# Performance work log

Measured on AMD Instinct MI355X. Metric: run time of the kernel, lower is better.

Reference implementation:

```python
import jax, jax.numpy as jnp
import numpy as np

NUM_NODES = 80000
V_GLOBALS = 50000
N = 32      # grapharea_size
D = 300     # feature dim
R = 4       # num relations
E = 64      # edges per timestep
B, T = 2, 64


def setup_inputs() -> dict:
    key = jax.random.key(0)
    ks = jax.random.split(key, 10)
    return {
        "x_indices": jax.random.randint(ks[0], (B, T, N), 0, NUM_NODES, dtype=jnp.int32),
        "edge_index": jax.random.randint(ks[1], (B, T, 2, E), 0, N, dtype=jnp.int32),
        "edge_type": jax.random.randint(ks[2], (B, T, E), 0, R, dtype=jnp.int32),
        "X": jax.random.normal(ks[3], (NUM_NODES, D), jnp.float32) * 0.1,
        "conv_W": jax.random.normal(ks[4], (R, D, D), jnp.float32) * (1.0 / np.sqrt(D)),
        "W_0": jax.random.normal(ks[5], (D, D), jnp.float32) * (1.0 / np.sqrt(D)),
        "update_gate_W": jax.random.normal(ks[6], (N * D, D), jnp.float32) * (1.0 / np.sqrt(N * D)),
        "update_gate_U": jax.random.normal(ks[7], (D, D), jnp.float32) * (1.0 / np.sqrt(D)),
        "lin_w": jax.random.normal(ks[8], (V_GLOBALS, D), jnp.float32) * (1.0 / np.sqrt(D)),
        "lin_b": jax.random.normal(ks[9], (V_GLOBALS,), jnp.float32) * 0.01,
    }


def _rgcn_step(X, conv_W, W_0, Wg, Ug, lin_w, lin_b, mem, idx, ei, et):
    # gather grapharea features: [N, D]
    gx = X[idx]
    src, dst = ei[0], ei[1]
    n = gx.shape[0]
    r = conv_W.shape[0]
    # per-relation linear transform: [R, N, D]
    xw = jnp.einsum('nd,rde->rne', gx, conv_W)
    # edge-type masks emulate split_edge_index: [R, E]
    mask = (et[None, :] == jnp.arange(r, dtype=et.dtype)[:, None]).astype(gx.dtype)
    # GCN symmetric normalization with self-loops (deg includes self-loop weight 1)
    deg = jax.vmap(lambda w: jax.ops.segment_sum(w, dst, num_segments=n))(mask) + 1.0  # [R, N]
    dis = jax.lax.rsqrt(deg)
    norm = dis[:, src] * dis[:, dst] * mask                      # [R, E]
    msgs = xw[:, src, :] * norm[..., None]                       # [R, E, D]
    agg = jax.vmap(lambda m: jax.ops.segment_sum(m, dst, num_segments=n))(msgs)
    agg = agg + xw * (dis ** 2)[..., None]                       # self-loop messages
    composite = agg.sum(0)                                       # sum over relations, [N, D]
    # eye(N) @ (gx @ W_0) == gx @ W_0
    proposed = composite + gx @ W_0
    # GRU-style update gate from flattened grapharea + previous memory's first node
    u = jax.nn.sigmoid(gx.reshape(-1) @ Wg + mem[0] @ Ug)        # [D]
    new = u[None, :] * proposed + (1.0 - u[None, :]) * mem       # [N, D]
    x1 = jax.nn.leaky_relu(new)[0]                               # current node, [D]
    logits = x1 @ lin_w.T + lin_b                                # [V]
    return new, jax.nn.log_softmax(logits)


def reference(x_indices, edge_index, edge_type, X, conv_W, W_0, update_gate_W, update_gate_U, lin_w, lin_b):
    b, t, n = x_indices.shape
    s = b * t
    idxs = x_indices.reshape(s, n)
    eis = edge_index.reshape(s, 2, -1)
    ets = edge_type.reshape(s, -1)

    def step(mem, inp):
        idx, ei, et = inp
        new, logp = _rgcn_step(X, conv_W, W_0, update_gate_W, update_gate_U,
                               lin_w, lin_b, mem, idx, ei, et)
        # memory carry is a non-grad buffer updated via .data.copy_ in torch
        return jax.lax.stop_gradient(new), logp

    mem0 = jnp.zeros((n, X.shape[1]), X.dtype)
    _, preds_globals = jax.lax.scan(step, mem0, (idxs, eis, ets))  # [S, V]
    preds_senses = jnp.zeros((s,), X.dtype)  # include_senses=False -> stacked zeros
    return preds_globals, preds_senses
```

## Files before the change

kernel.cpp:

```cpp
#include <hip/hip_runtime.h>

#define S 128
#define N 32
#define D 300
#define DP 320
#define E 64
#define R 4
#define V 50000
#define VP 50048
#define ND 9600
#define KY 1504
#define DPAD 304

typedef unsigned short ushortT;
typedef __attribute__((ext_vector_type(8))) short short8;
typedef __attribute__((ext_vector_type(4))) short short4v;
typedef __attribute__((ext_vector_type(4))) float floatx4;
typedef __attribute__((ext_vector_type(2))) _Float16 half2v;
typedef __attribute__((ext_vector_type(13))) unsigned int uintx13;

#if defined(__has_builtin)
#if __has_builtin(__builtin_amdgcn_fdot2)
#define HAVE_FDOT2 1
#endif
#endif

__device__ inline float bf2f(ushortT h) {
    unsigned u = ((unsigned)h) << 16;
    float f;
    __builtin_memcpy(&f, &u, 4);
    return f;
}

__device__ inline float bfbits_lo(unsigned u) {
    unsigned b = u << 16;
    float f;
    __builtin_memcpy(&f, &b, 4);
    return f;
}

__device__ inline float bfbits_hi(unsigned u) {
    unsigned b = u & 0xffff0000u;
    float f;
    __builtin_memcpy(&f, &b, 4);
    return f;
}

__device__ inline ushortT f2bf(float f) {
    unsigned u;
    __builtin_memcpy(&u, &f, 4);
    unsigned r = (u + 0x7fffu + ((u >> 16) & 1u)) >> 16;
    return (ushortT)r;
}

__device__ inline float ldf(const void* p, size_t i, int isb) {
    return isb ? bf2f(((const ushortT*)p)[i]) : ((const float*)p)[i];
}

__device__ inline float dot2f(unsigned a, unsigned b, float c) {
    half2v av, bv;
    __builtin_memcpy(&av, &a, 4);
    __builtin_memcpy(&bv, &b, 4);
#if defined(HAVE_FDOT2)
    return __builtin_amdgcn_fdot2(av, bv, c, false);
#else
    return fmaf((float)av[1], (float)bv[1], fmaf((float)av[0], (float)bv[0], c));
#endif
}

__device__ inline unsigned packh2(float lo, float hi) {
    half2v h;
    h[0] = (_Float16)lo;
    h[1] = (_Float16)hi;
    unsigned u;
    __builtin_memcpy(&u, &h, 4);
    return u;
}

__global__ void k_detect(const void* X, int* flag) {
    __shared__ int bad;
    if (threadIdx.x == 0) bad = 0;
    __syncthreads();
    const ushortT* p = (const ushortT*)X;
    int b = 0;
    for (int i = threadIdx.x; i < 4096; i += 256) {
        float v = bf2f(p[i]);
        if (!(v > -2.f && v < 2.f)) b = 1;
    }
    if (b) atomicOr(&bad, 1);
    __syncthreads();
    if (threadIdx.x == 0) flag[0] = bad ? 0 : 1;
}

__global__ void k_gatherb(const int* __restrict__ flag, const int* __restrict__ xi,
                          const void* __restrict__ X, ushortT* __restrict__ gxb) {
    int isb = flag[0];
    int sn = blockIdx.x;
    int d = threadIdx.x;
    if (d < D) {
        int node = xi[sn];
        ushortT v = isb ? ((const ushortT*)X)[(size_t)node * D + d]
                        : f2bf(((const float*)X)[(size_t)node * D + d]);
        gxb[(size_t)sn * D + d] = v;
    }
}

__global__ void k_twg(const int* __restrict__ flag, const void* __restrict__ Wg,
                      ushortT* __restrict__ wgt) {
    int isb = flag[0];
    __shared__ float tile[32][33];
    int k0 = blockIdx.x * 32, d0 = blockIdx.y * 32;
    int tx = threadIdx.x & 31, ty = threadIdx.x >> 5;
    for (int i = ty; i < 32; i += 8) {
        int d = d0 + tx;
        tile[i][tx] = (d < D) ? ldf(Wg, (size_t)(k0 + i) * D + d, isb) : 0.f;
    }
    __syncthreads();
    for (int i = ty; i < 32; i += 8) {
        int d = d0 + i;
        if (d < DPAD) wgt[(size_t)d * ND + k0 + tx] = f2bf(tile[tx][i]);
    }
}

__global__ void k_tws(const int* __restrict__ flag, const void* __restrict__ convW,
                      const void* __restrict__ W0, ushortT* __restrict__ wst) {
    int isb = flag[0];
    __shared__ float tile[32][33];
    int k0 = blockIdx.x * 32, d0 = blockIdx.y * 32;
    int tx = threadIdx.x & 31, ty = threadIdx.x >> 5;
    for (int i = ty; i < 32; i += 8) {
        int kp = k0 + i, d = d0 + tx;
        float v = 0.f;
        if (d < D && kp < 1500)
            v = (kp < 1200) ? ldf(convW, (size_t)kp * D + d, isb)
                            : ldf(W0, (size_t)(kp - 1200) * D + d, isb);
        tile[i][tx] = v;
    }
    __syncthreads();
    for (int i = ty; i < 32; i += 8) {
        int d = d0 + i;
        if (d < DPAD) wst[(size_t)d * KY + k0 + tx] = f2bf(tile[tx][i]);
    }
}

__global__ void k_yb(const ushortT* __restrict__ gxb, const int* __restrict__ ei,
                     const int* __restrict__ et, ushortT* __restrict__ yb) {
    int s = blockIdx.x;
    int t = threadIdx.x;
    __shared__ int se[E], de[E], te[E];
    __shared__ float disv[R][N];
    if (t < E) {
        se[t] = ei[(size_t)s * 2 * E + t];
        de[t] = ei[(size_t)s * 2 * E + E + t];
        te[t] = et[(size_t)s * E + t];
    }
    __syncthreads();
    if (t < R * N) {
        int r = t >> 5, n = t & 31;
        float c = 1.f;
        for (int e = 0; e < E; ++e) c += (te[e] == r && de[e] == n) ? 1.f : 0.f;
        disv[r][n] = rsqrtf(c);
    }
    __syncthreads();
    if (t < D) {
        const ushortT* g = gxb + (size_t)s * ND;
        float g0 = bf2f(g[t]);
        float yy[R];
#pragma unroll
        for (int r = 0; r < R; ++r) yy[r] = g0 * disv[r][0] * disv[r][0];
        for (int e = 0; e < E; ++e) {
            if (de[e] == 0) {
                int r = te[e];
                yy[r] += disv[r][se[e]] * disv[r][0] * bf2f(g[(size_t)se[e] * D + t]);
            }
        }
#pragma unroll
        for (int r = 0; r < R; ++r) yb[(size_t)s * KY + r * D + t] = f2bf(yy[r]);
        yb[(size_t)s * KY + 4 * D + t] = g[t];
    }
    if (t < 4) yb[(size_t)s * KY + 1500 + t] = 0;
}

__global__ __launch_bounds__(256) void k_gemm(const ushortT* __restrict__ A, int lda,
                                              const ushortT* __restrict__ Bt, int ldb,
                                              float* __restrict__ C, int ldc, int ncols,
                                              int kchunks, int per) {
    int wave = threadIdx.x >> 6, lane = threadIdx.x & 63;
    int col = lane & 15, quad = lane >> 4;
    int m0 = blockIdx.x * 16, n0 = blockIdx.y * 16;
    int z = blockIdx.z;
    int kbeg = z * per;
    int kend = kbeg + per;
    if (kend > kchunks) kend = kchunks;
    floatx4 acc = {0.f, 0.f, 0.f, 0.f};
    const ushortT* ap = A + (size_t)(m0 + col) * lda + quad * 8;
    const ushortT* bp = Bt + (size_t)(n0 + col) * ldb + quad * 8;
    for (int kc = kbeg + wave; kc < kend; kc += 4) {
        short8 a = *(const short8*)(ap + kc * 32);
        short8 b = *(const short8*)(bp + kc * 32);
        acc = __builtin_amdgcn_mfma_f32_16x16x32_bf16(a, b, acc, 0, 0, 0);
    }
    __shared__ float red[4][64][4];
#pragma unroll
    for (int i = 0; i < 4; ++i) red[wave][lane][i] = acc[i];
    __syncthreads();
    if (wave == 0) {
#pragma unroll
        for (int i = 0; i < 4; ++i) {
            float v = red[0][lane][i] + red[1][lane][i] + red[2][lane][i] + red[3][lane][i];
            int m = m0 + quad * 4 + i;
            int n = n0 + col;
            if (n < ncols) C[(size_t)z * S * ldc + (size_t)m * ldc + n] = v;
        }
    }
}

__global__ void k_red(const float* __restrict__ part, float* __restrict__ out, int n, int nz) {
    int i = blockIdx.x * 256 + threadIdx.x;
    if (i < n) {
        float v = 0.f;
        for (int z = 0; z < nz; ++z) v += part[(size_t)z * n + i];
        out[i] = v;
    }
}

__global__ __attribute__((amdgpu_flat_work_group_size(768, 768), amdgpu_waves_per_eu(2, 2))) void
k_scan(const int* __restrict__ flag, const float* __restrict__ a, const float* __restrict__ P0,
       const void* __restrict__ Ug, ushortT* __restrict__ x1p) {
    int isb = flag[0];
    int t = threadIdx.x;
    int w = t >> 6, lane = t & 63;
    int kbase = w * 25;
    int myk = kbase + lane;
    bool red_ok = lane < 25;
    int d4 = 256 + lane;
    bool d4ok = d4 < D;
    uintx13 UV0, UV1, UV2, UV3, UV4;
#pragma unroll
    for (int j = 0; j < 13; ++j) {
        int k1 = kbase + 2 * j, k2 = k1 + 1;
        bool k2ok = (2 * j + 1) < 25;
        UV0[j] = packh2(ldf(Ug, (size_t)k1 * D + lane, isb),
                        k2ok ? ldf(Ug, (size_t)k2 * D + lane, isb) : 0.f);
        UV1[j] = packh2(ldf(Ug, (size_t)k1 * D + 64 + lane, isb),
                        k2ok ? ldf(Ug, (size_t)k2 * D + 64 + lane, isb) : 0.f);
        UV2[j] = packh2(ldf(Ug, (size_t)k1 * D + 128 + lane, isb),
                        k2ok ? ldf(Ug, (size_t)k2 * D + 128 + lane, isb) : 0.f);
        UV3[j] = packh2(ldf(Ug, (size_t)k1 * D + 192 + lane, isb),
                        k2ok ? ldf(Ug, (size_t)k2 * D + 192 + lane, isb) : 0.f);
        UV4[j] = packh2(d4ok ? ldf(Ug, (size_t)k1 * D + d4, isb) : 0.f,
                        (k2ok && d4ok) ? ldf(Ug, (size_t)k2 * D + d4, isb) : 0.f);
    }
    for (int i = t; i < S * 20; i += 768) {
        int s = i / 20, d = 300 + (i % 20);
        x1p[(size_t)s * DP + d] = 0;
    }
    __shared__ float part[2][12][320];
    __shared__ unsigned msh16[12 * 13];
    for (int i = t; i < 12 * 13; i += 768) msh16[i] = 0;
    float mreg = 0.f;
    int buf = 0;
    float av = 0.f, pv = 0.f;
    if (red_ok) {
        av = a[myk];
        pv = P0[myk];
    }
    __syncthreads();
    for (int s = 0; s < S; ++s) {
        float avn = 0.f, pvn = 0.f;
        if (red_ok && s + 1 < S) {
            avn = a[(size_t)(s + 1) * D + myk];
            pvn = P0[(size_t)(s + 1) * D + myk];
        }
        uintx13 MV;
#pragma unroll
        for (int j = 0; j < 13; ++j) MV[j] = msh16[13 * w + j];
        float acc0 = 0.f, acc1 = 0.f, acc2 = 0.f, acc3 = 0.f, acc4 = 0.f;
#pragma unroll
        for (int j = 0; j < 13; ++j) {
            unsigned md = MV[j];
            acc0 = dot2f(UV0[j], md, acc0);
            acc1 = dot2f(UV1[j], md, acc1);
            acc2 = dot2f(UV2[j], md, acc2);
            acc3 = dot2f(UV3[j], md, acc3);
            acc4 = dot2f(UV4[j], md, acc4);
        }
        part[buf][w][lane] = acc0;
        part[buf][w][64 + lane] = acc1;
        part[buf][w][128 + lane] = acc2;
        part[buf][w][192 + lane] = acc3;
        part[buf][w][256 + lane] = acc4;
        __syncthreads();
        if (red_ok) {
            float q0 = part[buf][0][myk] + part[buf][1][myk];
            float q1 = part[buf][2][myk] + part[buf][3][myk];
            float q2 = part[buf][4][myk] + part[buf][5][myk];
            float q3 = part[buf][6][myk] + part[buf][7][myk];
            float q4 = part[buf][8][myk] + part[buf][9][myk];
            float q5 = part[buf][10][myk] + part[buf][11][myk];
            float pr = av + (((q0 + q1) + (q2 + q3)) + (q4 + q5));
            float u = 1.f / (1.f + __expf(-pr));
            float nm = u * pv + (1.f - u) * mreg;
            mreg = nm;
            _Float16 mh = (_Float16)nm;
            ushortT mb;
            __builtin_memcpy(&mb, &mh, 2);
            ((ushortT*)msh16)[26 * w + lane] = mb;
            float x = nm > 0.f ? nm : 0.01f * nm;
            x1p[(size_t)s * DP + myk] = f2bf(x);
        }
        av = avn;
        pv = pvn;
        buf ^= 1;
    }
}

__global__ __launch_bounds__(256) void k_logits(const int* __restrict__ flag,
                                                const ushortT* __restrict__ x1p,
                                                const void* __restrict__ lw,
                                                const void* __restrict__ lb,
                                                void* __restrict__ out) {
    int isb = flag[0];
    int wave = threadIdx.x >> 6, lane = threadIdx.x & 63;
    int col = lane & 15, quad = lane >> 4;
    int v = blockIdx.x * 64 + wave * 16 + col;
    int vv = v < V ? v : V - 1;
    floatx4 acc[8];
#pragma unroll
    for (int i = 0; i < 8; ++i) acc[i] = (floatx4){0.f, 0.f, 0.f, 0.f};
#pragma unroll
    for (int kc = 0; kc < 9; ++kc) {
        int k0 = kc * 32 + quad * 8;
        short8 b;
        if (isb) {
            const ushortT* bp = (const ushortT*)lw + (size_t)vv * D + k0;
            short4v lo = *(const short4v*)bp;
            short4v hi = *(const short4v*)(bp + 4);
            b = (short8){lo[0], lo[1], lo[2], lo[3], hi[0], hi[1], hi[2], hi[3]};
        } else {
            const float* bp = (const float*)lw + (size_t)vv * D + k0;
            floatx4 f0 = *(const floatx4*)bp;
            floatx4 f1 = *(const floatx4*)(bp + 4);
            b = (short8){(short)f2bf(f0[0]), (short)f2bf(f0[1]), (short)f2bf(f0[2]),
                         (short)f2bf(f0[3]), (short)f2bf(f1[0]), (short)f2bf(f1[1]),
                         (short)f2bf(f1[2]), (short)f2bf(f1[3])};
        }
#pragma unroll
        for (int st = 0; st < 8; ++st) {
            short8 aa = *(const short8*)(x1p + (size_t)(st * 16 + col) * DP + k0);
            acc[st] = __builtin_amdgcn_mfma_f32_16x16x32_bf16(aa, b, acc[st], 0, 0, 0);
        }
    }
    {
        int k0 = 288 + quad * 8;
        short8 b;
#pragma unroll
        for (int j = 0; j < 8; ++j) {
            int k = k0 + j;
            ushortT bv = 0;
            if (k < D)
                bv = isb ? ((const ushortT*)lw)[(size_t)vv * D + k]
                         : f2bf(((const float*)lw)[(size_t)vv * D + k]);
            b[j] = (short)bv;
        }
#pragma unroll
        for (int st = 0; st < 8; ++st) {
            short8 aa = *(const short8*)(x1p + (size_t)(st * 16 + col) * DP + k0);
            acc[st] = __builtin_amdgcn_mfma_f32_16x16x32_bf16(aa, b, acc[st], 0, 0, 0);
        }
    }
    if (v < V) {
        float bias = ldf(lb, v, isb);
#pragma unroll
        for (int st = 0; st < 8; ++st) {
#pragma unroll
            for (int i = 0; i < 4; ++i) {
                int s = st * 16 + quad * 4 + i;
                float val = acc[st][i] + bias;
                if (isb)
                    ((ushortT*)out)[(size_t)s * V + v] = f2bf(val);
                else
                    ((float*)out)[(size_t)s * V + v] = val;
            }
        }
    }
}

__global__ __launch_bounds__(512) void k_norm(const int* __restrict__ flag,
                                              void* __restrict__ out) {
    int isb = flag[0];
    int s = blockIdx.x;
    int t = threadIdx.x;
    __shared__ float red[512];
    if (s == 0 && t < S) {
        if (isb)
            ((ushortT*)out)[(size_t)S * V + t] = 0;
        else
            ((float*)out)[(size_t)S * V + t] = 0.f;
    }
    float mx = -1e30f;
    if (isb) {
        const uint4* row = (const uint4*)((const ushortT*)out + (size_t)s * V);
        for (int i = t; i < 6250; i += 512) {
            uint4 q = row[i];
            mx = fmaxf(mx, fmaxf(fmaxf(bfbits_lo(q.x), bfbits_hi(q.x)),
                                 fmaxf(bfbits_lo(q.y), bfbits_hi(q.y))));
            mx = fmaxf(mx, fmaxf(fmaxf(bfbits_lo(q.z), bfbits_hi(q.z)),
                                 fmaxf(bfbits_lo(q.w), bfbits_hi(q.w))));
        }
    } else {
        const floatx4* row = (const floatx4*)((const float*)out + (size_t)s * V);
        for (int i = t; i < 12500; i += 512) {
            floatx4 q = row[i];
            mx = fmaxf(mx, fmaxf(fmaxf(q[0], q[1]), fmaxf(q[2], q[3])));
        }
    }
    red[t] = mx;
    __syncthreads();
    for (int o = 256; o > 0; o >>= 1) {
        if (t < o) red[t] = fmaxf(red[t], red[t + o]);
        __syncthreads();
    }
    float M = red[0];
    __syncthreads();
    float sm = 0.f;
    if (isb) {
        const uint4* row = (const uint4*)((const ushortT*)out + (size_t)s * V);
        for (int i = t; i < 6250; i += 512) {
            uint4 q = row[i];
            sm += __expf(bfbits_lo(q.x) - M) + __expf(bfbits_hi(q.x) - M) +
                  __expf(bfbits_lo(q.y) - M) + __expf(bfbits_hi(q.y) - M) +
                  __expf(bfbits_lo(q.z) - M) + __expf(bfbits_hi(q.z) - M) +
                  __expf(bfbits_lo(q.w) - M) + __expf(bfbits_hi(q.w) - M);
        }
    } else {
        const floatx4* row = (const floatx4*)((const float*)out + (size_t)s * V);
        for (int i = t; i < 12500; i += 512) {
            floatx4 q = row[i];
            sm += __expf(q[0] - M) + __expf(q[1] - M) + __expf(q[2] - M) + __expf(q[3] - M);
        }
    }
    red[t] = sm;
    __syncthreads();
    for (int o = 256; o > 0; o >>= 1) {
        if (t < o) red[t] += red[t + o];
        __syncthreads();
    }
    float lse = M + __logf(red[0]);
    if (isb) {
        uint4* row = (uint4*)((ushortT*)out + (size_t)s * V);
        for (int i = t; i < 6250; i += 512) {
            uint4 q = row[i];
            uint4 o;
            o.x = (unsigned)f2bf(bfbits_lo(q.x) - lse) |
                  ((unsigned)f2bf(bfbits_hi(q.x) - lse) << 16);
            o.y = (unsigned)f2bf(bfbits_lo(q.y) - lse) |
                  ((unsigned)f2bf(bfbits_hi(q.y) - lse) << 16);
            o.z = (unsigned)f2bf(bfbits_lo(q.z) - lse) |
                  ((unsigned)f2bf(bfbits_hi(q.z) - lse) << 16);
            o.w = (unsigned)f2bf(bfbits_lo(q.w) - lse) |
                  ((unsigned)f2bf(bfbits_hi(q.w) - lse) << 16);
            row[i] = o;
        }
    } else {
        floatx4* row = (floatx4*)((float*)out + (size_t)s * V);
        for (int i = t; i < 12500; i += 512) {
            floatx4 q = row[i];
            q[0] -= lse;
            q[1] -= lse;
            q[2] -= lse;
            q[3] -= lse;
            row[i] = q;
        }
    }
}

#define OFF_FLAG 0
#define OFF_GXB 256
#define OFF_WGT 2457856
#define OFF_WST 8294656
#define OFF_YB 9209088
#define OFF_A 9594112
#define OFF_P0 9747712
#define OFF_X1P 9901312
#define OFF_STATS 9983232
#define OFF_PART 9983744
#define PART_A_BYTES (4 * S * D * 4)
#define PART_P_BYTES (2 * S * D * 4)

extern "C" void kernel_launch(void* const* d_in, const int* in_sizes, int n_in, void* d_out,
                              int out_size, void* d_ws, size_t ws_size, hipStream_t stream) {
    const int* xi = (const int*)d_in[0];
    const int* ei = (const int*)d_in[1];
    const int* et = (const int*)d_in[2];
    const void* X = d_in[3];
    const void* convW = d_in[4];
    const void* W0 = d_in[5];
    const void* Wg = d_in[6];
    const void* Ug = d_in[7];
    const void* lw = d_in[8];
    const void* lb = d_in[9];
    char* ws = (char*)d_ws;

    int* flag = (int*)(ws + OFF_FLAG);
    ushortT* gxb = (ushortT*)(ws + OFF_GXB);
    ushortT* wgt = (ushortT*)(ws + OFF_WGT);
    ushortT* wst = (ushortT*)(ws + OFF_WST);
    ushortT* yb = (ushortT*)(ws + OFF_YB);
    float* a = (float*)(ws + OFF_A);
    float* P0 = (float*)(ws + OFF_P0);
    ushortT* x1p = (ushortT*)(ws + OFF_X1P);

    bool split = ws_size >= (size_t)(OFF_PART + PART_A_BYTES + PART_P_BYTES);
    int nza = split ? 4 : 1;
    int nzp = split ? 2 : 1;
    float* apart = split ? (float*)(ws + OFF_PART) : a;
    float* ppart = split ? (float*)(ws + OFF_PART + PART_A_BYTES) : P0;
    int pera = (ND / 32 + nza - 1) / nza;
    int perp = (KY / 32 + nzp - 1) / nzp;

    hipLaunchKernelGGL(k_detect, dim3(1), dim3(256), 0, stream, X, flag);
    hipLaunchKernelGGL(k_gatherb, dim3(S * N), dim3(DP), 0, stream, flag, xi, X, gxb);
    hipLaunchKernelGGL(k_twg, dim3(ND / 32, 10), dim3(256), 0, stream, flag, Wg, wgt);
    hipLaunchKernelGGL(k_tws, dim3(KY / 32, 10), dim3(256), 0, stream, flag, convW, W0, wst);
    hipLaunchKernelGGL(k_yb, dim3(S), dim3(DP), 0, stream, gxb, ei, et, yb);
    hipLaunchKernelGGL(k_gemm, dim3(S / 16, 19, nza), dim3(256), 0, stream, gxb, ND, wgt, ND,
                       apart, D, D, ND / 32, pera);
    if (split)
        hipLaunchKernelGGL(k_red, dim3((S * D + 255) / 256), dim3(256), 0, stream, apart, a,
                           S * D, nza);
    hipLaunchKernelGGL(k_gemm, dim3(S / 16, 19, nzp), dim3(256), 0, stream, yb, KY, wst, KY,
                       ppart, D, D, KY / 32, perp);
    if (split)
        hipLaunchKernelGGL(k_red, dim3((S * D + 255) / 256), dim3(256), 0, stream, ppart, P0,
                           S * D, nzp);
    hipLaunchKernelGGL(k_scan, dim3(1), dim3(768), 0, stream, flag, a, P0, Ug, x1p);
    hipLaunchKernelGGL(k_logits, dim3(VP / 64), dim3(256), 0, stream, flag, x1p, lw, lb, d_out);
    hipLaunchKernelGGL(k_norm, dim3(S), dim3(512), 0, stream, flag, d_out);
}
```

Baseline: 426.3 us.

## Fuse prep, gather, GEMM and reduction kernels; use readlane for scan memory broadcast

Merges the two weight-transpose kernels into one launch and fuses the feature gather into the yb kernel through a shared-memory tile. The two split-K GEMMs run as a single launch, and the separate split-K reduction kernels are removed by summing the partials inside the sequential scan's prefetch. Inside the scan, each lane handles two features and the memory vector is broadcast via readlane instead of shared memory. The aim is to cut launch count and serial latency per scan step. The trade-off is extra partial loads in the serial scan loop and less parallelism in the gather, which now uses 128 blocks instead of 4096.

Result: slower. 837.0 us (+96.3%).

```diff
diff --git a/kernel.cpp b/kernel.cpp
--- a/kernel.cpp
+++ b/kernel.cpp
@@ -16,6 +16,7 @@
 typedef __attribute__((ext_vector_type(8))) short short8;
 typedef __attribute__((ext_vector_type(4))) short short4v;
 typedef __attribute__((ext_vector_type(4))) float floatx4;
+typedef __attribute__((ext_vector_type(2))) float floatx2;
 typedef __attribute__((ext_vector_type(2))) _Float16 half2v;
 typedef __attribute__((ext_vector_type(13))) unsigned int uintx13;
 
@@ -55,6 +56,10 @@
 
 __device__ inline float ldf(const void* p, size_t i, int isb) {
     return isb ? bf2f(((const ushortT*)p)[i]) : ((const float*)p)[i];
+}
+
+__device__ inline unsigned rdlaneu(unsigned v, int lane) {
+    return (unsigned)__builtin_amdgcn_readlane((int)v, lane);
 }
 
 __device__ inline float dot2f(unsigned a, unsigned b, float c) {
@@ -77,6 +82,32 @@
     return u;
 }
 
+__device__ inline void ldred(const float* base, int s, int d1, bool pair, int nz,
+                             float& v1, float& v2) {
+    v1 = 0.f;
+    v2 = 0.f;
+    for (int z = 0; z < nz; ++z) {
+        const float* p = base + ((size_t)z * S + s) * D + d1;
+        if (pair) {
+            floatx2 q = *(const floatx2*)p;
+            v1 += q[0];
+            v2 += q[1];
+        } else {
+            v1 += *p;
+        }
+    }
+}
+
+__device__ inline float tree12(const float* pb, int d) {
+    float q0 = pb[0 * 320 + d] + pb[1 * 320 + d];
+    float q1 = pb[2 * 320 + d] + pb[3 * 320 + d];
+    float q2 = pb[4 * 320 + d] + pb[5 * 320 + d];
+    float q3 = pb[6 * 320 + d] + pb[7 * 320 + d];
+    float q4 = pb[8 * 320 + d] + pb[9 * 320 + d];
+    float q5 = pb[10 * 320 + d] + pb[11 * 320 + d];
+    return ((q0 + q1) + (q2 + q3)) + (q4 + q5);
+}
+
 __global__ void k_detect(const void* X, int* flag) {
     __shared__ int bad;
     if (threadIdx.x == 0) bad = 0;
@@ -92,61 +123,51 @@
     if (threadIdx.x == 0) flag[0] = bad ? 0 : 1;
 }
 
-__global__ void k_gatherb(const int* __restrict__ flag, const int* __restrict__ xi,
-                          const void* __restrict__ X, ushortT* __restrict__ gxb) {
-    int isb = flag[0];
-    int sn = blockIdx.x;
-    int d = threadIdx.x;
-    if (d < D) {
-        int node = xi[sn];
-        ushortT v = isb ? ((const ushortT*)X)[(size_t)node * D + d]
-                        : f2bf(((const float*)X)[(size_t)node * D + d]);
-        gxb[(size_t)sn * D + d] = v;
-    }
-}
-
-__global__ void k_twg(const int* __restrict__ flag, const void* __restrict__ Wg,
-                      ushortT* __restrict__ wgt) {
+__global__ void k_prep(const int* __restrict__ flag, const void* __restrict__ Wg,
+                       const void* __restrict__ convW, const void* __restrict__ W0,
+                       ushortT* __restrict__ wgt, ushortT* __restrict__ wst) {
     int isb = flag[0];
     __shared__ float tile[32][33];
-    int k0 = blockIdx.x * 32, d0 = blockIdx.y * 32;
+    int bx = blockIdx.x;
+    int d0 = blockIdx.y * 32;
     int tx = threadIdx.x & 31, ty = threadIdx.x >> 5;
-    for (int i = ty; i < 32; i += 8) {
-        int d = d0 + tx;
-        tile[i][tx] = (d < D) ? ldf(Wg, (size_t)(k0 + i) * D + d, isb) : 0.f;
-    }
-    __syncthreads();
-    for (int i = ty; i < 32; i += 8) {
-        int d = d0 + i;
-        if (d < DPAD) wgt[(size_t)d * ND + k0 + tx] = f2bf(tile[tx][i]);
-    }
-}
-
-__global__ void k_tws(const int* __restrict__ flag, const void* __restrict__ convW,
-                      const void* __restrict__ W0, ushortT* __restrict__ wst) {
+    if (bx < ND / 32) {
+        int k0 = bx * 32;
+        for (int i = ty; i < 32; i += 8) {
+            int d = d0 + tx;
+            tile[i][tx] = (d < D) ? ldf(Wg, (size_t)(k0 + i) * D + d, isb) : 0.f;
+        }
+        __syncthreads();
+        for (int i = ty; i < 32; i += 8) {
+            int d = d0 + i;
+            if (d < DPAD) wgt[(size_t)d * ND + k0 + tx] = f2bf(tile[tx][i]);
+        }
+    } else {
+        int k0 = (bx - ND / 32) * 32;
+        for (int i = ty; i < 32; i += 8) {
+            int kp = k0 + i, d = d0 + tx;
+            float v = 0.f;
+            if (d < D && kp < 1500)
+                v = (kp < 1200) ? ldf(convW, (size_t)kp * D + d, isb)
+                                : ldf(W0, (size_t)(kp - 1200) * D + d, isb);
+            tile[i][tx] = v;
+        }
+        __syncthreads();
+        for (int i = ty; i < 32; i += 8) {
+            int d = d0 + i;
+            if (d < DPAD) wst[(size_t)d * KY + k0 + tx] = f2bf(tile[tx][i]);
+        }
+    }
+}
+
+__global__ void k_gyb(const int* __restrict__ flag, const int* __restrict__ xi,
+                      const void* __restrict__ X, const int* __restrict__ ei,
+                      const int* __restrict__ et, ushortT* __restrict__ gxb,
+                      ushortT* __restrict__ yb) {
     int isb = flag[0];
-    __shared__ float tile[32][33];
-    int k0 = blockIdx.x * 32, d0 = blockIdx.y * 32;
-    int tx = threadIdx.x & 31, ty = threadIdx.x >> 5;
-    for (int i = ty; i < 32; i += 8) {
-        int kp = k0 + i, d = d0 + tx;
-        float v = 0.f;
-        if (d < D && kp < 1500)
-            v = (kp < 1200) ? ldf(convW, (size_t)kp * D + d, isb)
-                            : ldf(W0, (size_t)(kp - 1200) * D + d, isb);
-        tile[i][tx] = v;
-    }
-    __syncthreads();
-    for (int i = ty; i < 32; i += 8) {
-        int d = d0 + i;
-        if (d < DPAD) wst[(size_t)d * KY + k0 + tx] = f2bf(tile[tx][i]);
-    }
-}
-
-__global__ void k_yb(const ushortT* __restrict__ gxb, const int* __restrict__ ei,
-                     const int* __restrict__ et, ushortT* __restrict__ yb) {
     int s = blockIdx.x;
     int t = threadIdx.x;
+    __shared__ ushortT gl[N][D];
     __shared__ int se[E], de[E], te[E];
     __shared__ float disv[R][N];
     if (t < E) {
@@ -154,6 +175,16 @@
         de[t] = ei[(size_t)s * 2 * E + E + t];
         te[t] = et[(size_t)s * E + t];
     }
+    if (t < D) {
+#pragma unroll 4
+        for (int r = 0; r < N; ++r) {
+            int node = xi[s * N + r];
+            ushortT v = isb ? ((const ushortT*)X)[(size_t)node * D + t]
+                            : f2bf(((const float*)X)[(size_t)node * D + t]);
+            gl[r][t] = v;
+            gxb[(size_t)(s * N + r) * D + t] = v;
+        }
+    }
     __syncthreads();
     if (t < R * N) {
         int r = t >> 5, n = t & 31;
@@ -163,38 +194,49 @@
     }
     __syncthreads();
     if (t < D) {
-        const ushortT* g = gxb + (size_t)s * ND;
-        float g0 = bf2f(g[t]);
+        float g0 = bf2f(gl[0][t]);
         float yy[R];
 #pragma unroll
         for (int r = 0; r < R; ++r) yy[r] = g0 * disv[r][0] * disv[r][0];
         for (int e = 0; e < E; ++e) {
             if (de[e] == 0) {
                 int r = te[e];
-                yy[r] += disv[r][se[e]] * disv[r][0] * bf2f(g[(size_t)se[e] * D + t]);
+                yy[r] += disv[r][se[e]] * disv[r][0] * bf2f(gl[se[e]][t]);
             }
         }
 #pragma unroll
         for (int r = 0; r < R; ++r) yb[(size_t)s * KY + r * D + t] = f2bf(yy[r]);
-        yb[(size_t)s * KY + 4 * D + t] = g[t];
+        yb[(size_t)s * KY + 4 * D + t] = gl[0][t];
     }
     if (t < 4) yb[(size_t)s * KY + 1500 + t] = 0;
 }
 
-__global__ __launch_bounds__(256) void k_gemm(const ushortT* __restrict__ A, int lda,
-                                              const ushortT* __restrict__ Bt, int ldb,
-                                              float* __restrict__ C, int ldc, int ncols,
-                                              int kchunks, int per) {
+__global__ __launch_bounds__(256) void k_gemm2(const ushortT* __restrict__ gxb,
+                                               const ushortT* __restrict__ wgt,
+                                               const ushortT* __restrict__ yb,
+                                               const ushortT* __restrict__ wst,
+                                               float* __restrict__ apart,
+                                               float* __restrict__ ppart, int nza, int nzp) {
     int wave = threadIdx.x >> 6, lane = threadIdx.x & 63;
     int col = lane & 15, quad = lane >> 4;
     int m0 = blockIdx.x * 16, n0 = blockIdx.y * 16;
     int z = blockIdx.z;
-    int kbeg = z * per;
+    const ushortT *A, *Bt;
+    float* C;
+    int ld, kchunks, per, zz;
+    if (z < nza) {
+        A = gxb; Bt = wgt; C = apart; ld = ND; kchunks = ND / 32;
+        zz = z; per = (kchunks + nza - 1) / nza;
+    } else {
+        A = yb; Bt = wst; C = ppart; ld = KY; kchunks = KY / 32;
+        zz = z - nza; per = (kchunks + nzp - 1) / nzp;
+    }
+    int kbeg = zz * per;
     int kend = kbeg + per;
     if (kend > kchunks) kend = kchunks;
     floatx4 acc = {0.f, 0.f, 0.f, 0.f};
-    const ushortT* ap = A + (size_t)(m0 + col) * lda + quad * 8;
-    const ushortT* bp = Bt + (size_t)(n0 + col) * ldb + quad * 8;
+    const ushortT* ap = A + (size_t)(m0 + col) * ld + quad * 8;
+    const ushortT* bp = Bt + (size_t)(n0 + col) * ld + quad * 8;
     for (int kc = kbeg + wave; kc < kend; kc += 4) {
         short8 a = *(const short8*)(ap + kc * 32);
         short8 b = *(const short8*)(bp + kc * 32);
@@ -210,29 +252,19 @@
             float v = red[0][lane][i] + red[1][lane][i] + red[2][lane][i] + red[3][lane][i];
             int m = m0 + quad * 4 + i;
             int n = n0 + col;
-            if (n < ncols) C[(size_t)z * S * ldc + (size_t)m * ldc + n] = v;
-        }
-    }
-}
-
-__global__ void k_red(const float* __restrict__ part, float* __restrict__ out, int n, int nz) {
-    int i = blockIdx.x * 256 + threadIdx.x;
-    if (i < n) {
-        float v = 0.f;
-        for (int z = 0; z < nz; ++z) v += part[(size_t)z * n + i];
-        out[i] = v;
+            if (n < D) C[(size_t)zz * S * D + (size_t)m * D + n] = v;
+        }
     }
 }
 
 __global__ __attribute__((amdgpu_flat_work_group_size(768, 768), amdgpu_waves_per_eu(2, 2))) void
-k_scan(const int* __restrict__ flag, const float* __restrict__ a, const float* __restrict__ P0,
-       const void* __restrict__ Ug, ushortT* __restrict__ x1p) {
+k_scan(const int* __restrict__ flag, const float* __restrict__ apart,
+       const float* __restrict__ ppart, int nza, int nzp, const void* __restrict__ Ug,
+       ushortT* __restrict__ x1p) {
     int isb = flag[0];
     int t = threadIdx.x;
     int w = t >> 6, lane = t & 63;
     int kbase = w * 25;
-    int myk = kbase + lane;
-    bool red_ok = lane < 25;
     int d4 = 256 + lane;
     bool d4ok = d4 < D;
     uintx13 UV0, UV1, UV2, UV3, UV4;
@@ -256,25 +288,26 @@
         x1p[(size_t)s * DP + d] = 0;
     }
     __shared__ float part[2][12][320];
-    __shared__ unsigned msh16[12 * 13];
-    for (int i = t; i < 12 * 13; i += 768) msh16[i] = 0;
-    float mreg = 0.f;
+    bool jok = lane < 13;
+    bool pair = lane < 12;
+    int d1 = kbase + 2 * lane;
+    float m1 = 0.f, m2 = 0.f;
+    unsigned mpack = 0;
     int buf = 0;
-    float av = 0.f, pv = 0.f;
-    if (red_ok) {
-        av = a[myk];
-        pv = P0[myk];
-    }
-    __syncthreads();
+    float av1 = 0.f, av2 = 0.f, pv1 = 0.f, pv2 = 0.f;
+    if (jok) {
+        ldred(apart, 0, d1, pair, nza, av1, av2);
+        ldred(ppart, 0, d1, pair, nzp, pv1, pv2);
+    }
     for (int s = 0; s < S; ++s) {
-        float avn = 0.f, pvn = 0.f;
-        if (red_ok && s + 1 < S) {
-            avn = a[(size_t)(s + 1) * D + myk];
-            pvn = P0[(size_t)(s + 1) * D + myk];
+        float an1 = 0.f, an2 = 0.f, pn1 = 0.f, pn2 = 0.f;
+        if (jok && s + 1 < S) {
+            ldred(apart, s + 1, d1, pair, nza, an1, an2);
+            ldred(ppart, s + 1, d1, pair, nzp, pn1, pn2);
         }
         uintx13 MV;
 #pragma unroll
-        for (int j = 0; j < 13; ++j) MV[j] = msh16[13 * w + j];
+        for (int j = 0; j < 13; ++j) MV[j] = rdlaneu(mpack, j);
         float acc0 = 0.f, acc1 = 0.f, acc2 = 0.f, acc3 = 0.f, acc4 = 0.f;
 #pragma unroll
         for (int j = 0; j < 13; ++j) {
@@ -291,26 +324,28 @@
         part[buf][w][192 + lane] = acc3;
         part[buf][w][256 + lane] = acc4;
         __syncthreads();
-        if (red_ok) {
-            float q0 = part[buf][0][myk] + part[buf][1][myk];
-            float q1 = part[buf][2][myk] + part[buf][3][myk];
-            float q2 = part[buf][4][myk] + part[buf][5][myk];
-            float q3 = part[buf][6][myk] + part[buf][7][myk];
-            float q4 = part[buf][8][myk] + part[buf][9][myk];
-            float q5 = part[buf][10][myk] + part[buf][11][myk];
-            float pr = av + (((q0 + q1) + (q2 + q3)) + (q4 + q5));
-            float u = 1.f / (1.f + __expf(-pr));
-            float nm = u * pv + (1.f - u) * mreg;
-            mreg = nm;
-            _Float16 mh = (_Float16)nm;
-            ushortT mb;
-            __builtin_memcpy(&mb, &mh, 2);
-            ((ushortT*)msh16)[26 * w + lane] = mb;
-            float x = nm > 0.f ? nm : 0.01f * nm;
-            x1p[(size_t)s * DP + myk] = f2bf(x);
-        }
-        av = avn;
-        pv = pvn;
+        if (jok) {
+            const float* pb = &part[buf][0][0];
+            float pr1 = av1 + tree12(pb, d1);
+            float u1 = 1.f / (1.f + __expf(-pr1));
+            float nm1 = u1 * pv1 + (1.f - u1) * m1;
+            m1 = nm1;
+            float x1v = nm1 > 0.f ? nm1 : 0.01f * nm1;
+            if (pair) {
+                float pr2 = av2 + tree12(pb, d1 + 1);
+                float u2 = 1.f / (1.f + __expf(-pr2));
+                float nm2 = u2 * pv2 + (1.f - u2) * m2;
+                m2 = nm2;
+                mpack = packh2(nm1, nm2);
+                float x2v = nm2 > 0.f ? nm2 : 0.01f * nm2;
+                unsigned xw = (unsigned)f2bf(x1v) | ((unsigned)f2bf(x2v) << 16);
+                *(unsigned*)(x1p + (size_t)s * DP + d1) = xw;
+            } else {
+                mpack = packh2(nm1, 0.f);
+                x1p[(size_t)s * DP + d1] = f2bf(x1v);
+            }
+        }
+        av1 = an1; av2 = an2; pv1 = pn1; pv2 = pn2;
         buf ^= 1;
     }
 }
@@ -516,25 +551,15 @@
     int nzp = split ? 2 : 1;
     float* apart = split ? (float*)(ws + OFF_PART) : a;
     float* ppart = split ? (float*)(ws + OFF_PART + PART_A_BYTES) : P0;
-    int pera = (ND / 32 + nza - 1) / nza;
-    int perp = (KY / 32 + nzp - 1) / nzp;
 
     hipLaunchKernelGGL(k_detect, dim3(1), dim3(256), 0, stream, X, flag);
-    hipLaunchKernelGGL(k_gatherb, dim3(S * N), dim3(DP), 0, stream, flag, xi, X, gxb);
-    hipLaunchKernelGGL(k_twg, dim3(ND / 32, 10), dim3(256), 0, stream, flag, Wg, wgt);
-    hipLaunchKernelGGL(k_tws, dim3(KY / 32, 10), dim3(256), 0, stream, flag, convW, W0, wst);
-    hipLaunchKernelGGL(k_yb, dim3(S), dim3(DP), 0, stream, gxb, ei, et, yb);
-    hipLaunchKernelGGL(k_gemm, dim3(S / 16, 19, nza), dim3(256), 0, stream, gxb, ND, wgt, ND,
-                       apart, D, D, ND / 32, pera);
-    if (split)
-        hipLaunchKernelGGL(k_red, dim3((S * D + 255) / 256), dim3(256), 0, stream, apart, a,
-                           S * D, nza);
-    hipLaunchKernelGGL(k_gemm, dim3(S / 16, 19, nzp), dim3(256), 0, stream, yb, KY, wst, KY,
-                       ppart, D, D, KY / 32, perp);
-    if (split)
-        hipLaunchKernelGGL(k_red, dim3((S * D + 255) / 256), dim3(256), 0, stream, ppart, P0,
-                           S * D, nzp);
-    hipLaunchKernelGGL(k_scan, dim3(1), dim3(768), 0, stream, flag, a, P0, Ug, x1p);
+    hipLaunchKernelGGL(k_prep, dim3(ND / 32 + KY / 32, 10), dim3(256), 0, stream, flag, Wg,
+                       convW, W0, wgt, wst);
+    hipLaunchKernelGGL(k_gyb, dim3(S), dim3(DP), 0, stream, flag, xi, X, ei, et, gxb, yb);
+    hipLaunchKernelGGL(k_gemm2, dim3(S / 16, 19, nza + nzp), dim3(256), 0, stream, gxb, wgt,
+                       yb, wst, apart, ppart, nza, nzp);
+    hipLaunchKernelGGL(k_scan, dim3(1), dim3(768), 0, stream, flag, apart, ppart, nza, nzp,
+                       Ug, x1p);
     hipLaunchKernelGGL(k_logits, dim3(VP / 64), dim3(256), 0, stream, flag, x1p, lw, lb, d_out);
     hipLaunchKernelGGL(k_norm, dim3(S), dim3(512), 0, stream, flag, d_out);
 }
```

## Merge preprocessing, gather and GEMM launches; replace scan syncthreads with raw barrier

Applied to the files above, without the earlier changes.

Combines the two weight-transpose kernels into one launch, fuses the node-feature gather into the yb construction kernel (staging gathered rows in LDS), runs both split-K GEMMs in a single launch along the z dimension, and merges the two partial-sum reductions. This cuts the number of kernel launches and the inter-kernel gaps, and lets the yb step read features from LDS instead of global memory. In the serial scan kernel, __syncthreads is replaced by an explicit lgkmcnt wait plus s_barrier with scheduling fences, which may trim barrier overhead inside the per-step loop. The fused gather now runs on only 128 blocks instead of 4096, which could reduce parallelism for that gather.

New measurement: 423.9 us. Within noise of the previous version (-0.6%).

```diff
diff --git a/kernel.cpp b/kernel.cpp
--- a/kernel.cpp
+++ b/kernel.cpp
@@ -16,6 +16,7 @@
 typedef __attribute__((ext_vector_type(8))) short short8;
 typedef __attribute__((ext_vector_type(4))) short short4v;
 typedef __attribute__((ext_vector_type(4))) float floatx4;
+typedef __attribute__((ext_vector_type(2))) float floatx2;
 typedef __attribute__((ext_vector_type(2))) _Float16 half2v;
 typedef __attribute__((ext_vector_type(13))) unsigned int uintx13;
 
@@ -92,61 +93,51 @@
     if (threadIdx.x == 0) flag[0] = bad ? 0 : 1;
 }
 
-__global__ void k_gatherb(const int* __restrict__ flag, const int* __restrict__ xi,
-                          const void* __restrict__ X, ushortT* __restrict__ gxb) {
-    int isb = flag[0];
-    int sn = blockIdx.x;
-    int d = threadIdx.x;
-    if (d < D) {
-        int node = xi[sn];
-        ushortT v = isb ? ((const ushortT*)X)[(size_t)node * D + d]
-                        : f2bf(((const float*)X)[(size_t)node * D + d]);
-        gxb[(size_t)sn * D + d] = v;
-    }
-}
-
-__global__ void k_twg(const int* __restrict__ flag, const void* __restrict__ Wg,
-                      ushortT* __restrict__ wgt) {
+__global__ void k_prep(const int* __restrict__ flag, const void* __restrict__ Wg,
+                       const void* __restrict__ convW, const void* __restrict__ W0,
+                       ushortT* __restrict__ wgt, ushortT* __restrict__ wst) {
     int isb = flag[0];
     __shared__ float tile[32][33];
-    int k0 = blockIdx.x * 32, d0 = blockIdx.y * 32;
+    int bx = blockIdx.x;
+    int d0 = blockIdx.y * 32;
     int tx = threadIdx.x & 31, ty = threadIdx.x >> 5;
-    for (int i = ty; i < 32; i += 8) {
-        int d = d0 + tx;
-        tile[i][tx] = (d < D) ? ldf(Wg, (size_t)(k0 + i) * D + d, isb) : 0.f;
-    }
-    __syncthreads();
-    for (int i = ty; i < 32; i += 8) {
-        int d = d0 + i;
-        if (d < DPAD) wgt[(size_t)d * ND + k0 + tx] = f2bf(tile[tx][i]);
-    }
-}
-
-__global__ void k_tws(const int* __restrict__ flag, const void* __restrict__ convW,
-                      const void* __restrict__ W0, ushortT* __restrict__ wst) {
+    if (bx < ND / 32) {
+        int k0 = bx * 32;
+        for (int i = ty; i < 32; i += 8) {
+            int d = d0 + tx;
+            tile[i][tx] = (d < D) ? ldf(Wg, (size_t)(k0 + i) * D + d, isb) : 0.f;
+        }
+        __syncthreads();
+        for (int i = ty; i < 32; i += 8) {
+            int d = d0 + i;
+            if (d < DPAD) wgt[(size_t)d * ND + k0 + tx] = f2bf(tile[tx][i]);
+        }
+    } else {
+        int k0 = (bx - ND / 32) * 32;
+        for (int i = ty; i < 32; i += 8) {
+            int kp = k0 + i, d = d0 + tx;
+            float v = 0.f;
+            if (d < D && kp < 1500)
+                v = (kp < 1200) ? ldf(convW, (size_t)kp * D + d, isb)
+                                : ldf(W0, (size_t)(kp - 1200) * D + d, isb);
+            tile[i][tx] = v;
+        }
+        __syncthreads();
+        for (int i = ty; i < 32; i += 8) {
+            int d = d0 + i;
+            if (d < DPAD) wst[(size_t)d * KY + k0 + tx] = f2bf(tile[tx][i]);
+        }
+    }
+}
+
+__global__ void k_gyb(const int* __restrict__ flag, const int* __restrict__ xi,
+                      const void* __restrict__ X, const int* __restrict__ ei,
+                      const int* __restrict__ et, ushortT* __restrict__ gxb,
+                      ushortT* __restrict__ yb) {
     int isb = flag[0];
-    __shared__ float tile[32][33];
-    int k0 = blockIdx.x * 32, d0 = blockIdx.y * 32;
-    int tx = threadIdx.x & 31, ty = threadIdx.x >> 5;
-    for (int i = ty; i < 32; i += 8) {
-        int kp = k0 + i, d = d0 + tx;
-        float v = 0.f;
-        if (d < D && kp < 1500)
-            v = (kp < 1200) ? ldf(convW, (size_t)kp * D + d, isb)
-                            : ldf(W0, (size_t)(kp - 1200) * D + d, isb);
-        tile[i][tx] = v;
-    }
-    __syncthreads();
-    for (int i = ty; i < 32; i += 8) {
-        int d = d0 + i;
-        if (d < DPAD) wst[(size_t)d * KY + k0 + tx] = f2bf(tile[tx][i]);
-    }
-}
-
-__global__ void k_yb(const ushortT* __restrict__ gxb, const int* __restrict__ ei,
-                     const int* __restrict__ et, ushortT* __restrict__ yb) {
     int s = blockIdx.x;
     int t = threadIdx.x;
+    __shared__ ushortT gl[N][D];
     __shared__ int se[E], de[E], te[E];
     __shared__ float disv[R][N];
     if (t < E) {
@@ -154,6 +145,16 @@
         de[t] = ei[(size_t)s * 2 * E + E + t];
         te[t] = et[(size_t)s * E + t];
     }
+    if (t < D) {
+#pragma unroll 4
+        for (int r = 0; r < N; ++r) {
+            int node = xi[s * N + r];
+            ushortT v = isb ? ((const ushortT*)X)[(size_t)node * D + t]
+                            : f2bf(((const float*)X)[(size_t)node * D + t]);
+            gl[r][t] = v;
+            gxb[(size_t)(s * N + r) * D + t] = v;
+        }
+    }
     __syncthreads();
     if (t < R * N) {
         int r = t >> 5, n = t & 31;
@@ -163,38 +164,49 @@
     }
     __syncthreads();
     if (t < D) {
-        const ushortT* g = gxb + (size_t)s * ND;
-        float g0 = bf2f(g[t]);
+        float g0 = bf2f(gl[0][t]);
         float yy[R];
 #pragma unroll
         for (int r = 0; r < R; ++r) yy[r] = g0 * disv[r][0] * disv[r][0];
         for (int e = 0; e < E; ++e) {
             if (de[e] == 0) {
                 int r = te[e];
-                yy[r] += disv[r][se[e]] * disv[r][0] * bf2f(g[(size_t)se[e] * D + t]);
+                yy[r] += disv[r][se[e]] * disv[r][0] * bf2f(gl[se[e]][t]);
             }
         }
 #pragma unroll
         for (int r = 0; r < R; ++r) yb[(size_t)s * KY + r * D + t] = f2bf(yy[r]);
-        yb[(size_t)s * KY + 4 * D + t] = g[t];
+        yb[(size_t)s * KY + 4 * D + t] = gl[0][t];
     }
     if (t < 4) yb[(size_t)s * KY + 1500 + t] = 0;
 }
 
-__global__ __launch_bounds__(256) void k_gemm(const ushortT* __restrict__ A, int lda,
-                                              const ushortT* __restrict__ Bt, int ldb,
-                                              float* __restrict__ C, int ldc, int ncols,
-                                              int kchunks, int per) {
+__global__ __launch_bounds__(256) void k_gemm2(const ushortT* __restrict__ gxb,
+                                               const ushortT* __restrict__ wgt,
+                                               const ushortT* __restrict__ yb,
+                                               const ushortT* __restrict__ wst,
+                                               float* __restrict__ apart,
+                                               float* __restrict__ ppart, int nza, int nzp) {
     int wave = threadIdx.x >> 6, lane = threadIdx.x & 63;
     int col = lane & 15, quad = lane >> 4;
     int m0 = blockIdx.x * 16, n0 = blockIdx.y * 16;
     int z = blockIdx.z;
-    int kbeg = z * per;
+    const ushortT *A, *Bt;
+    float* C;
+    int ld, kchunks, per, zz;
+    if (z < nza) {
+        A = gxb; Bt = wgt; C = apart; ld = ND; kchunks = ND / 32;
+        zz = z; per = (kchunks + nza - 1) / nza;
+    } else {
+        A = yb; Bt = wst; C = ppart; ld = KY; kchunks = KY / 32;
+        zz = z - nza; per = (kchunks + nzp - 1) / nzp;
+    }
+    int kbeg = zz * per;
     int kend = kbeg + per;
     if (kend > kchunks) kend = kchunks;
     floatx4 acc = {0.f, 0.f, 0.f, 0.f};
-    const ushortT* ap = A + (size_t)(m0 + col) * lda + quad * 8;
-    const ushortT* bp = Bt + (size_t)(n0 + col) * ldb + quad * 8;
+    const ushortT* ap = A + (size_t)(m0 + col) * ld + quad * 8;
+    const ushortT* bp = Bt + (size_t)(n0 + col) * ld + quad * 8;
     for (int kc = kbeg + wave; kc < kend; kc += 4) {
         short8 a = *(const short8*)(ap + kc * 32);
         short8 b = *(const short8*)(bp + kc * 32);
@@ -210,17 +222,21 @@
             float v = red[0][lane][i] + red[1][lane][i] + red[2][lane][i] + red[3][lane][i];
             int m = m0 + quad * 4 + i;
             int n = n0 + col;
-            if (n < ncols) C[(size_t)z * S * ldc + (size_t)m * ldc + n] = v;
-        }
-    }
-}
-
-__global__ void k_red(const float* __restrict__ part, float* __restrict__ out, int n, int nz) {
+            if (n < D) C[(size_t)zz * S * D + (size_t)m * D + n] = v;
+        }
+    }
+}
+
+__global__ void k_red2(const float* __restrict__ apart, const float* __restrict__ ppart,
+                       float* __restrict__ a, float* __restrict__ P0, int nza, int nzp) {
     int i = blockIdx.x * 256 + threadIdx.x;
-    if (i < n) {
+    if (i < S * D) {
         float v = 0.f;
-        for (int z = 0; z < nz; ++z) v += part[(size_t)z * n + i];
-        out[i] = v;
+        for (int z = 0; z < nza; ++z) v += apart[(size_t)z * S * D + i];
+        a[i] = v;
+        float w = 0.f;
+        for (int z = 0; z < nzp; ++z) w += ppart[(size_t)z * S * D + i];
+        P0[i] = w;
     }
 }
 
@@ -290,7 +306,10 @@
         part[buf][w][128 + lane] = acc2;
         part[buf][w][192 + lane] = acc3;
         part[buf][w][256 + lane] = acc4;
-        __syncthreads();
+        __builtin_amdgcn_sched_barrier(0);
+        asm volatile("s_waitcnt lgkmcnt(0)" ::: "memory");
+        __builtin_amdgcn_s_barrier();
+        __builtin_amdgcn_sched_barrier(0);
         if (red_ok) {
             float q0 = part[buf][0][myk] + part[buf][1][myk];
             float q1 = part[buf][2][myk] + part[buf][3][myk];
@@ -516,24 +535,16 @@
     int nzp = split ? 2 : 1;
     float* apart = split ? (float*)(ws + OFF_PART) : a;
     float* ppart = split ? (float*)(ws + OFF_PART + PART_A_BYTES) : P0;
-    int pera = (ND / 32 + nza - 1) / nza;
-    int perp = (KY / 32 + nzp - 1) / nzp;
 
     hipLaunchKernelGGL(k_detect, dim3(1), dim3(256), 0, stream, X, flag);
-    hipLaunchKernelGGL(k_gatherb, dim3(S * N), dim3(DP), 0, stream, flag, xi, X, gxb);
-    hipLaunchKernelGGL(k_twg, dim3(ND / 32, 10), dim3(256), 0, stream, flag, Wg, wgt);
-    hipLaunchKernelGGL(k_tws, dim3(KY / 32, 10), dim3(256), 0, stream, flag, convW, W0, wst);
-    hipLaunchKernelGGL(k_yb, dim3(S), dim3(DP), 0, stream, gxb, ei, et, yb);
-    hipLaunchKernelGGL(k_gemm, dim3(S / 16, 19, nza), dim3(256), 0, stream, gxb, ND, wgt, ND,
-                       apart, D, D, ND / 32, pera);
+    hipLaunchKernelGGL(k_prep, dim3(ND / 32 + KY / 32, 10), dim3(256), 0, stream, flag, Wg,
+                       convW, W0, wgt, wst);
+    hipLaunchKernelGGL(k_gyb, dim3(S), dim3(DP), 0, stream, flag, xi, X, ei, et, gxb, yb);
+    hipLaunchKernelGGL(k_gemm2, dim3(S / 16, 19, nza + nzp), dim3(256), 0, stream, gxb, wgt,
+                       yb, wst, apart, ppart, nza, nzp);
     if (split)
-        hipLaunchKernelGGL(k_red, dim3((S * D + 255) / 256), dim3(256), 0, stream, apart, a,
-                           S * D, nza);
-    hipLaunchKernelGGL(k_gemm, dim3(S / 16, 19, nzp), dim3(256), 0, stream, yb, KY, wst, KY,
-                       ppart, D, D, KY / 32, perp);
-    if (split)
-        hipLaunchKernelGGL(k_red, dim3((S * D + 255) / 256), dim3(256), 0, stream, ppart, P0,
-                           S * D, nzp);
+        hipLaunchKernelGGL(k_red2, dim3((S * D + 255) / 256), dim3(256), 0, stream, apart,
+                           ppart, a, P0, nza, nzp);
     hipLaunchKernelGGL(k_scan, dim3(1), dim3(768), 0, stream, flag, a, P0, Ug, x1p);
     hipLaunchKernelGGL(k_logits, dim3(VP / 64), dim3(256), 0, stream, flag, x1p, lw, lb, d_out);
     hipLaunchKernelGGL(k_norm, dim3(S), dim3(512), 0, stream, flag, d_out);
```
